# Optimization experiments

Hardware: AMD Instinct MI355X
Metric: run time of the kernel (lower is better)

Reference implementation:

```python
import jax, jax.numpy as jnp
import numpy as np
from jax import lax

B_SZ, L, D, N = 4, 2048, 768, 16


def setup_inputs() -> dict:
    key = jax.random.key(0)
    ks = jax.random.split(key, 8)
    x = jax.random.normal(ks[0], (B_SZ, L, D), dtype=jnp.float32)
    # A_log init: log(repeat(arange(1, N+1), 'n -> d n'))
    A_log = jnp.log(jnp.tile(jnp.arange(1, N + 1, dtype=jnp.float32), (D, 1)))  # (D, N)
    sD = 1.0 / np.sqrt(D)
    Wb = jax.random.normal(ks[1], (N, D), dtype=jnp.float32) * sD
    bb = jax.random.normal(ks[2], (N,), dtype=jnp.float32) * sD
    Wc = jax.random.normal(ks[3], (N, D), dtype=jnp.float32) * sD
    bc = jax.random.normal(ks[4], (N,), dtype=jnp.float32) * sD
    W1 = jax.random.normal(ks[5], (1, D), dtype=jnp.float32) * sD
    b1 = jnp.zeros((1,), dtype=jnp.float32)
    Wd = jax.random.normal(ks[6], (D, 1), dtype=jnp.float32)
    bd = jax.random.normal(ks[7], (D,), dtype=jnp.float32)
    return {"x": x, "A_log": A_log, "Wb": Wb, "bb": bb, "Wc": Wc, "bc": bc,
            "W1": W1, "b1": b1, "Wd": Wd, "bd": bd}


def reference(x, A_log, Wb, bb, Wc, bc, W1, b1, Wd, bd):
    # x: (b, l, d)
    A = -jnp.exp(A_log)                                   # (d, n)
    Bp = x @ Wb.T + bb                                    # (b, l, n)
    C = x @ Wc.T + bc                                     # (b, l, n)
    s1 = x @ W1.T + b1                                    # (b, l, 1)
    delta = jax.nn.softplus(s1 @ Wd.T + bd)               # (b, l, d)
    deltaA = jnp.exp(jnp.einsum('bld,dn->bldn', delta, A))          # (b, l, d, n)
    deltaB_u = jnp.einsum('bld,bln,bld->bldn', delta, Bp, x)        # (b, l, d, n)

    def step(h, inputs):
        dA, dBu, c = inputs                               # (b,d,n),(b,d,n),(b,n)
        h = dA * h + dBu
        y = jnp.einsum('bdn,bn->bd', h, c)
        return h, y

    b, l, d = x.shape
    n = A_log.shape[1]
    h0 = jnp.zeros((b, d, n), dtype=x.dtype)
    _, ys = lax.scan(step, h0, (jnp.moveaxis(deltaA, 1, 0),
                                jnp.moveaxis(deltaB_u, 1, 0),
                                jnp.moveaxis(C, 1, 0)))
    return jnp.moveaxis(ys, 0, 1)                          # (b, l, d)
```

## Files before the change

kernel.cpp:

```cpp
#include <hip/hip_runtime.h>
#include <math.h>

#define B_SZ 4
#define LSEQ 2048
#define DDIM 768
#define NST  16
#define NROW (B_SZ * LSEQ)
#define NJ   33

#define KSPLIT 16
#define KCHUNK (DDIM / KSPLIT)

__global__ __launch_bounds__(256) void proj_part_kernel(
    const float* __restrict__ x,
    const float* __restrict__ Wb, const float* __restrict__ Wc,
    const float* __restrict__ W1, float* __restrict__ part)
{
    __shared__ float xs[256 * (KCHUNK + 1)];
    const int tid = threadIdx.x;
    const int row0 = blockIdx.x * 256;
    const int s = blockIdx.y;
    const int k0 = s * KCHUNK;

    for (int i = tid; i < 256 * (KCHUNK / 4); i += 256) {
        const int r = i / (KCHUNK / 4);
        const int kq = i % (KCHUNK / 4);
        const float4 v = *(const float4*)(x + (size_t)(row0 + r) * DDIM + k0 + kq * 4);
        float* dst = xs + r * (KCHUNK + 1) + kq * 4;
        dst[0] = v.x; dst[1] = v.y; dst[2] = v.z; dst[3] = v.w;
    }
    __syncthreads();

    float xr[KCHUNK];
    #pragma unroll
    for (int k = 0; k < KCHUNK; ++k) xr[k] = xs[tid * (KCHUNK + 1) + k];

    float acc[NJ];
    #pragma unroll
    for (int j = 0; j < NJ; ++j) acc[j] = 0.f;

    #pragma unroll
    for (int j = 0; j < NJ; ++j) {
        const float* wr = (j < 16) ? (Wb + j * DDIM)
                        : (j < 32) ? (Wc + (j - 16) * DDIM)
                                   : W1;
        const float* wk = wr + k0;
        #pragma unroll
        for (int k = 0; k < KCHUNK; ++k) acc[j] = fmaf(xr[k], wk[k], acc[j]);
    }
    #pragma unroll
    for (int j = 0; j < NJ; ++j)
        part[((size_t)s * NJ + j) * NROW + row0 + tid] = acc[j];
}

__global__ __launch_bounds__(256) void proj_reduce_kernel(
    const float* __restrict__ part,
    const float* __restrict__ bb, const float* __restrict__ bc,
    const float* __restrict__ b1,
    float* __restrict__ Bp, float* __restrict__ Cc, float* __restrict__ s1)
{
    const int idx = blockIdx.x * 256 + threadIdx.x;
    const int j = idx / NROW;
    const int row = idx % NROW;
    float a = 0.f;
    #pragma unroll
    for (int s = 0; s < KSPLIT; ++s)
        a += part[((size_t)s * NJ + j) * NROW + row];
    if (j < 16)      Bp[(size_t)row * NST + j] = a + bb[j];
    else if (j < 32) Cc[(size_t)row * NST + (j - 16)] = a + bc[j - 16];
    else             s1[row] = a + b1[0];
}

__device__ __forceinline__ float softplus_f(float z) {
    float t = __expf(-fabsf(z));
    return fmaxf(z, 0.f) + __logf(1.f + t);
}

__device__ __forceinline__ void powers16(float p, float* e) {
    e[0] = p;      e[1] = p * p;      e[2] = e[1] * p;   e[3] = e[1] * e[1];
    e[4] = e[3] * p;  e[5] = e[3] * e[1];  e[6] = e[3] * e[2];  e[7] = e[3] * e[3];
    e[8] = e[7] * p;  e[9] = e[7] * e[1];  e[10] = e[7] * e[2]; e[11] = e[7] * e[3];
    e[12] = e[7] * e[4]; e[13] = e[7] * e[5]; e[14] = e[7] * e[6]; e[15] = e[7] * e[7];
}

__device__ __forceinline__ bool a_structured(const float* acoef) {
    bool st = true;
    #pragma unroll
    for (int n = 0; n < NST; ++n)
        st = st && (fabsf(acoef[n] - (float)(n + 1) * acoef[0]) <= 1e-5f * fabsf(acoef[n]));
    return __all(st) != 0;
}

template <int CS>
__global__ __launch_bounds__(256) void pass1_kernel(
    const float* __restrict__ x, const float* __restrict__ A_log,
    const float* __restrict__ Wd, const float* __restrict__ bd,
    const float* __restrict__ Bp, const float* __restrict__ s1,
    float* __restrict__ Ssum, float* __restrict__ Q)
{
    const int tid = threadIdx.x;
    const int d = blockIdx.x * 256 + tid;
    const int c = blockIdx.y, b = blockIdx.z;
    const int NC = gridDim.y;
    const int rowbase = b * LSEQ + c * CS;

    const float wd = Wd[d], bdv = bd[d];
    float acoef[NST];
    #pragma unroll
    for (int n = 0; n < NST; ++n) acoef[n] = -__expf(A_log[d * NST + n]);
    const float a0 = acoef[0];
    const bool structured = a_structured(acoef);

    const float4* B4 = (const float4*)(Bp + (size_t)rowbase * NST);
    const float* s1p = s1 + rowbase;
    const float* xp = x + (size_t)rowbase * DDIM + d;

    float h[NST];
    #pragma unroll
    for (int n = 0; n < NST; ++n) h[n] = 0.f;
    float S = 0.f;

    if (structured) {
        #pragma unroll 4
        for (int l = 0; l < CS; ++l) {
            const float delta = softplus_f(fmaf(s1p[l], wd, bdv));
            S += delta;
            float e[NST];
            powers16(__expf(delta * a0), e);
            const float dx = delta * xp[(size_t)l * DDIM];
            const float4 b0 = B4[l * 4 + 0], b1v = B4[l * 4 + 1];
            const float4 b2 = B4[l * 4 + 2], b3v = B4[l * 4 + 3];
            const float bv[NST] = {b0.x, b0.y, b0.z, b0.w, b1v.x, b1v.y, b1v.z, b1v.w,
                                   b2.x, b2.y, b2.z, b2.w, b3v.x, b3v.y, b3v.z, b3v.w};
            #pragma unroll
            for (int n = 0; n < NST; ++n) h[n] = fmaf(e[n], h[n], dx * bv[n]);
        }
    } else {
        #pragma unroll 4
        for (int l = 0; l < CS; ++l) {
            const float delta = softplus_f(fmaf(s1p[l], wd, bdv));
            S += delta;
            float e[NST];
            #pragma unroll
            for (int n = 0; n < NST; ++n) e[n] = __expf(delta * acoef[n]);
            const float dx = delta * xp[(size_t)l * DDIM];
            const float4 b0 = B4[l * 4 + 0], b1v = B4[l * 4 + 1];
            const float4 b2 = B4[l * 4 + 2], b3v = B4[l * 4 + 3];
            const float bv[NST] = {b0.x, b0.y, b0.z, b0.w, b1v.x, b1v.y, b1v.z, b1v.w,
                                   b2.x, b2.y, b2.z, b2.w, b3v.x, b3v.y, b3v.z, b3v.w};
            #pragma unroll
            for (int n = 0; n < NST; ++n) h[n] = fmaf(e[n], h[n], dx * bv[n]);
        }
    }
    Ssum[((size_t)b * NC + c) * DDIM + d] = S;
    const size_t gbase = (((size_t)b * NC + c) * DDIM + d) * NST;
    float4* Q4 = (float4*)(Q + gbase);
    #pragma unroll
    for (int q = 0; q < 4; ++q)
        Q4[q] = make_float4(h[q * 4], h[q * 4 + 1], h[q * 4 + 2], h[q * 4 + 3]);
}

__global__ __launch_bounds__(64) void combine_kernel(
    const float* __restrict__ A_log,
    const float* __restrict__ Ssum, const float* __restrict__ Q,
    float* __restrict__ Hin, int NC)
{
    const int idx = blockIdx.x * 64 + threadIdx.x;
    const int b = idx / (DDIM * NST);
    const int r = idx % (DDIM * NST);
    const int d = r / NST;
    const float acoef = -__expf(A_log[r]);
    float h = 0.f;
    #pragma unroll 4
    for (int c = 0; c < NC; ++c) {
        const size_t base = (size_t)(b * NC + c);
        const float Sg = Ssum[base * DDIM + d];
        const float qg = Q[base * (DDIM * NST) + r];
        Hin[base * (DDIM * NST) + r] = h;
        h = fmaf(__expf(acoef * Sg), h, qg);
    }
}

template <int CS>
__global__ __launch_bounds__(256) void pass2_kernel(
    const float* __restrict__ x, const float* __restrict__ A_log,
    const float* __restrict__ Wd, const float* __restrict__ bd,
    const float* __restrict__ Bp, const float* __restrict__ Cc,
    const float* __restrict__ s1, const float* __restrict__ Hin,
    float* __restrict__ out)
{
    const int tid = threadIdx.x;
    const int d = blockIdx.x * 256 + tid;
    const int c = blockIdx.y, b = blockIdx.z;
    const int NC = gridDim.y;
    const int rowbase = b * LSEQ + c * CS;

    const float wd = Wd[d], bdv = bd[d];
    float acoef[NST];
    #pragma unroll
    for (int n = 0; n < NST; ++n) acoef[n] = -__expf(A_log[d * NST + n]);
    const float a0 = acoef[0];
    const bool structured = a_structured(acoef);

    const float4* B4 = (const float4*)(Bp + (size_t)rowbase * NST);
    const float4* C4 = (const float4*)(Cc + (size_t)rowbase * NST);
    const float* s1p = s1 + rowbase;
    const float* xp = x + (size_t)rowbase * DDIM + d;
    float* yp = out + (size_t)rowbase * DDIM + d;

    float h[NST];
    const size_t gbase = (((size_t)b * NC + c) * DDIM + d) * NST;
    const float4* H4 = (const float4*)(Hin + gbase);
    #pragma unroll
    for (int q = 0; q < 4; ++q) {
        const float4 hv = H4[q];
        h[q * 4] = hv.x; h[q * 4 + 1] = hv.y; h[q * 4 + 2] = hv.z; h[q * 4 + 3] = hv.w;
    }

    if (structured) {
        #pragma unroll 4
        for (int l = 0; l < CS; ++l) {
            const float delta = softplus_f(fmaf(s1p[l], wd, bdv));
            float e[NST];
            powers16(__expf(delta * a0), e);
            const float dx = delta * xp[(size_t)l * DDIM];
            const float4 b0 = B4[l * 4 + 0], b1v = B4[l * 4 + 1];
            const float4 b2 = B4[l * 4 + 2], b3v = B4[l * 4 + 3];
            const float4 c0 = C4[l * 4 + 0], c1v = C4[l * 4 + 1];
            const float4 c2 = C4[l * 4 + 2], c3v = C4[l * 4 + 3];
            const float bv[NST] = {b0.x, b0.y, b0.z, b0.w, b1v.x, b1v.y, b1v.z, b1v.w,
                                   b2.x, b2.y, b2.z, b2.w, b3v.x, b3v.y, b3v.z, b3v.w};
            const float cv[NST] = {c0.x, c0.y, c0.z, c0.w, c1v.x, c1v.y, c1v.z, c1v.w,
                                   c2.x, c2.y, c2.z, c2.w, c3v.x, c3v.y, c3v.z, c3v.w};
            float y = 0.f;
            #pragma unroll
            for (int n = 0; n < NST; ++n) {
                h[n] = fmaf(e[n], h[n], dx * bv[n]);
                y = fmaf(h[n], cv[n], y);
            }
            yp[(size_t)l * DDIM] = y;
        }
    } else {
        #pragma unroll 4
        for (int l = 0; l < CS; ++l) {
            const float delta = softplus_f(fmaf(s1p[l], wd, bdv));
            float e[NST];
            #pragma unroll
            for (int n = 0; n < NST; ++n) e[n] = __expf(delta * acoef[n]);
            const float dx = delta * xp[(size_t)l * DDIM];
            const float4 b0 = B4[l * 4 + 0], b1v = B4[l * 4 + 1];
            const float4 b2 = B4[l * 4 + 2], b3v = B4[l * 4 + 3];
            const float4 c0 = C4[l * 4 + 0], c1v = C4[l * 4 + 1];
            const float4 c2 = C4[l * 4 + 2], c3v = C4[l * 4 + 3];
            const float bv[NST] = {b0.x, b0.y, b0.z, b0.w, b1v.x, b1v.y, b1v.z, b1v.w,
                                   b2.x, b2.y, b2.z, b2.w, b3v.x, b3v.y, b3v.z, b3v.w};
            const float cv[NST] = {c0.x, c0.y, c0.z, c0.w, c1v.x, c1v.y, c1v.z, c1v.w,
                                   c2.x, c2.y, c2.z, c2.w, c3v.x, c3v.y, c3v.z, c3v.w};
            float y = 0.f;
            #pragma unroll
            for (int n = 0; n < NST; ++n) {
                h[n] = fmaf(e[n], h[n], dx * bv[n]);
                y = fmaf(h[n], cv[n], y);
            }
            yp[(size_t)l * DDIM] = y;
        }
    }
}

extern "C" void kernel_launch(void* const* d_in, const int* in_sizes, int n_in,
                              void* d_out, int out_size, void* d_ws, size_t ws_size,
                              hipStream_t stream) {
    const float* x     = (const float*)d_in[0];
    const float* A_log = (const float*)d_in[1];
    const float* Wb    = (const float*)d_in[2];
    const float* bb    = (const float*)d_in[3];
    const float* Wc    = (const float*)d_in[4];
    const float* bc    = (const float*)d_in[5];
    const float* W1    = (const float*)d_in[6];
    const float* b1    = (const float*)d_in[7];
    const float* Wd    = (const float*)d_in[8];
    const float* bd    = (const float*)d_in[9];
    float* out = (float*)d_out;

    float* ws = (float*)d_ws;
    const size_t partN = (size_t)KSPLIT * NJ * NROW;
    const size_t BpN = (size_t)NROW * NST;
    const size_t s1N = (size_t)NROW;

    int NC = 64;
    while (NC > 16) {
        size_t agg_ = (size_t)B_SZ * NC * DDIM * NST;
        size_t sN_ = (size_t)B_SZ * NC * DDIM;
        size_t need = (partN + 2 * BpN + s1N + sN_ + 2 * agg_) * sizeof(float);
        if (need <= ws_size) break;
        NC >>= 1;
    }
    const int CS = LSEQ / NC;

    float* part = ws;
    float* Bp   = part + partN;
    float* Cc   = Bp + BpN;
    float* s1   = Cc + BpN;
    float* Ssum = s1 + s1N;
    const size_t sN = (size_t)B_SZ * NC * DDIM;
    const size_t agg = (size_t)B_SZ * NC * DDIM * NST;
    float* Q    = Ssum + sN;
    float* Hin  = Q + agg;

    dim3 gproj(NROW / 256, KSPLIT);
    proj_part_kernel<<<gproj, 256, 0, stream>>>(x, Wb, Wc, W1, part);
    proj_reduce_kernel<<<(NJ * NROW) / 256, 256, 0, stream>>>(part, bb, bc, b1, Bp, Cc, s1);

    dim3 gscan(DDIM / 256, NC, B_SZ);
    if (CS == 32)
        pass1_kernel<32><<<gscan, 256, 0, stream>>>(x, A_log, Wd, bd, Bp, s1, Ssum, Q);
    else if (CS == 64)
        pass1_kernel<64><<<gscan, 256, 0, stream>>>(x, A_log, Wd, bd, Bp, s1, Ssum, Q);
    else
        pass1_kernel<128><<<gscan, 256, 0, stream>>>(x, A_log, Wd, bd, Bp, s1, Ssum, Q);

    combine_kernel<<<(B_SZ * DDIM * NST) / 64, 64, 0, stream>>>(A_log, Ssum, Q, Hin, NC);

    if (CS == 32)
        pass2_kernel<32><<<gscan, 256, 0, stream>>>(x, A_log, Wd, bd, Bp, Cc, s1, Hin, out);
    else if (CS == 64)
        pass2_kernel<64><<<gscan, 256, 0, stream>>>(x, A_log, Wd, bd, Bp, Cc, s1, Hin, out);
    else
        pass2_kernel<128><<<gscan, 256, 0, stream>>>(x, A_log, Wd, bd, Bp, Cc, s1, Hin, out);
}
```

Baseline: 160.6 us.

## Restructure projection GEMM split and parallelize chunk-carry combine with wave shuffles

The projection kernel now uses 64-row tiles with a 4-way K split, and each wave computes a subset of the 33 output columns. Before, each thread held 48 x values and all 33 accumulators, so register pressure was high and the partial-sum buffer was large. The combine kernel splits the 64 chunks across 4 lane groups, computes group products and carries, scans them with shuffles, and then writes Hin. This replaces a serial 64-step loop per state. The number of chunks is also fixed at 64 at compile time, which drops the workspace-size fallback and the template dispatch, so a smaller workspace would no longer be handled.

```diff
diff --git a/kernel.cpp b/kernel.cpp
--- a/kernel.cpp
+++ b/kernel.cpp
@@ -8,49 +8,63 @@
 #define NROW (B_SZ * LSEQ)
 #define NJ   33
 
-#define KSPLIT 16
-#define KCHUNK (DDIM / KSPLIT)
+#define NC   64
+#define CS   (LSEQ / NC)
+
+#define RB    64
+#define KSPL  4
+#define KC    (DDIM / KSPL)
 
 __global__ __launch_bounds__(256) void proj_part_kernel(
     const float* __restrict__ x,
     const float* __restrict__ Wb, const float* __restrict__ Wc,
     const float* __restrict__ W1, float* __restrict__ part)
 {
-    __shared__ float xs[256 * (KCHUNK + 1)];
+    __shared__ float xs[RB * (KC + 1)];
     const int tid = threadIdx.x;
-    const int row0 = blockIdx.x * 256;
+    const int row0 = blockIdx.x * RB;
     const int s = blockIdx.y;
-    const int k0 = s * KCHUNK;
-
-    for (int i = tid; i < 256 * (KCHUNK / 4); i += 256) {
-        const int r = i / (KCHUNK / 4);
-        const int kq = i % (KCHUNK / 4);
+    const int k0 = s * KC;
+
+    for (int i = tid; i < RB * (KC / 4); i += 256) {
+        const int r = i / (KC / 4);
+        const int kq = i % (KC / 4);
         const float4 v = *(const float4*)(x + (size_t)(row0 + r) * DDIM + k0 + kq * 4);
-        float* dst = xs + r * (KCHUNK + 1) + kq * 4;
+        float* dst = xs + r * (KC + 1) + kq * 4;
         dst[0] = v.x; dst[1] = v.y; dst[2] = v.z; dst[3] = v.w;
     }
     __syncthreads();
 
-    float xr[KCHUNK];
-    #pragma unroll
-    for (int k = 0; k < KCHUNK; ++k) xr[k] = xs[tid * (KCHUNK + 1) + k];
-
-    float acc[NJ];
-    #pragma unroll
-    for (int j = 0; j < NJ; ++j) acc[j] = 0.f;
-
-    #pragma unroll
-    for (int j = 0; j < NJ; ++j) {
+    const int row = tid & 63;
+    const int jg = __builtin_amdgcn_readfirstlane(tid >> 6);
+
+    const float* wp[9];
+    #pragma unroll
+    for (int t = 0; t < 9; ++t) {
+        const int j = 4 * t + jg;
         const float* wr = (j < 16) ? (Wb + j * DDIM)
                         : (j < 32) ? (Wc + (j - 16) * DDIM)
                                    : W1;
-        const float* wk = wr + k0;
+        wp[t] = wr + k0;
+    }
+    float acc[9];
+    #pragma unroll
+    for (int t = 0; t < 9; ++t) acc[t] = 0.f;
+
+    const float* xr = xs + row * (KC + 1);
+    #pragma unroll 8
+    for (int k = 0; k < KC; ++k) {
+        const float xv = xr[k];
         #pragma unroll
-        for (int k = 0; k < KCHUNK; ++k) acc[j] = fmaf(xr[k], wk[k], acc[j]);
-    }
-    #pragma unroll
-    for (int j = 0; j < NJ; ++j)
-        part[((size_t)s * NJ + j) * NROW + row0 + tid] = acc[j];
+        for (int t = 0; t < 9; ++t)
+            if (4 * t + jg < 33) acc[t] = fmaf(xv, wp[t][k], acc[t]);
+    }
+    #pragma unroll
+    for (int t = 0; t < 9; ++t) {
+        const int j = 4 * t + jg;
+        if (j < 33)
+            part[((size_t)s * NJ + j) * NROW + row0 + row] = acc[t];
+    }
 }
 
 __global__ __launch_bounds__(256) void proj_reduce_kernel(
@@ -64,7 +78,7 @@
     const int row = idx % NROW;
     float a = 0.f;
     #pragma unroll
-    for (int s = 0; s < KSPLIT; ++s)
+    for (int s = 0; s < KSPL; ++s)
         a += part[((size_t)s * NJ + j) * NROW + row];
     if (j < 16)      Bp[(size_t)row * NST + j] = a + bb[j];
     else if (j < 32) Cc[(size_t)row * NST + (j - 16)] = a + bc[j - 16];
@@ -91,7 +105,6 @@
     return __all(st) != 0;
 }
 
-template <int CS>
 __global__ __launch_bounds__(256) void pass1_kernel(
     const float* __restrict__ x, const float* __restrict__ A_log,
     const float* __restrict__ Wd, const float* __restrict__ bd,
@@ -101,7 +114,6 @@
     const int tid = threadIdx.x;
     const int d = blockIdx.x * 256 + tid;
     const int c = blockIdx.y, b = blockIdx.z;
-    const int NC = gridDim.y;
     const int rowbase = b * LSEQ + c * CS;
 
     const float wd = Wd[d], bdv = bd[d];
@@ -160,28 +172,54 @@
         Q4[q] = make_float4(h[q * 4], h[q * 4 + 1], h[q * 4 + 2], h[q * 4 + 3]);
 }
 
-__global__ __launch_bounds__(64) void combine_kernel(
+#define CPG (NC / 4)
+__global__ __launch_bounds__(256) void combine_kernel(
     const float* __restrict__ A_log,
     const float* __restrict__ Ssum, const float* __restrict__ Q,
-    float* __restrict__ Hin, int NC)
-{
-    const int idx = blockIdx.x * 64 + threadIdx.x;
-    const int b = idx / (DDIM * NST);
-    const int r = idx % (DDIM * NST);
-    const int d = r / NST;
+    float* __restrict__ Hin)
+{
+    const int gidx = blockIdx.x * 256 + threadIdx.x;
+    const int lane = threadIdx.x & 63;
+    const int rlow = gidx & 15;
+    const int g = (gidx >> 4) & 3;
+    const int hi = gidx >> 6;
+    const int pairIdx = hi * 16 + rlow;
+    const int b = pairIdx / (DDIM * NST);
+    const int r = pairIdx % (DDIM * NST);
+    const int d = r >> 4;
     const float acoef = -__expf(A_log[r]);
-    float h = 0.f;
-    #pragma unroll 4
-    for (int c = 0; c < NC; ++c) {
-        const size_t base = (size_t)(b * NC + c);
-        const float Sg = Ssum[base * DDIM + d];
-        const float qg = Q[base * (DDIM * NST) + r];
+    const int c0 = g * CPG;
+
+    float eq[CPG], qq[CPG];
+    #pragma unroll
+    for (int ci = 0; ci < CPG; ++ci) {
+        const size_t base = (size_t)(b * NC + c0 + ci);
+        eq[ci] = __expf(acoef * Ssum[base * DDIM + d]);
+        qq[ci] = Q[base * (DDIM * NST) + r];
+    }
+    float E = 1.f, H = 0.f;
+    #pragma unroll
+    for (int ci = 0; ci < CPG; ++ci) { H = fmaf(eq[ci], H, qq[ci]); E *= eq[ci]; }
+
+    float oE = __shfl_up(E, 16, 64);
+    float oH = __shfl_up(H, 16, 64);
+    if (lane >= 16) { H = fmaf(E, oH, H); E *= oE; }
+    oE = __shfl_up(E, 32, 64);
+    oH = __shfl_up(H, 32, 64);
+    if (lane >= 32) { H = fmaf(E, oH, H); E *= oE; }
+
+    float hin = __shfl_up(H, 16, 64);
+    if (g == 0) hin = 0.f;
+
+    float h = hin;
+    #pragma unroll
+    for (int ci = 0; ci < CPG; ++ci) {
+        const size_t base = (size_t)(b * NC + c0 + ci);
         Hin[base * (DDIM * NST) + r] = h;
-        h = fmaf(__expf(acoef * Sg), h, qg);
-    }
-}
-
-template <int CS>
+        h = fmaf(eq[ci], h, qq[ci]);
+    }
+}
+
 __global__ __launch_bounds__(256) void pass2_kernel(
     const float* __restrict__ x, const float* __restrict__ A_log,
     const float* __restrict__ Wd, const float* __restrict__ bd,
@@ -192,7 +230,6 @@
     const int tid = threadIdx.x;
     const int d = blockIdx.x * 256 + tid;
     const int c = blockIdx.y, b = blockIdx.z;
-    const int NC = gridDim.y;
     const int rowbase = b * LSEQ + c * CS;
 
     const float wd = Wd[d], bdv = bd[d];
@@ -283,48 +320,28 @@
     float* out = (float*)d_out;
 
     float* ws = (float*)d_ws;
-    const size_t partN = (size_t)KSPLIT * NJ * NROW;
+    const size_t partN = (size_t)KSPL * NJ * NROW;
     const size_t BpN = (size_t)NROW * NST;
     const size_t s1N = (size_t)NROW;
-
-    int NC = 64;
-    while (NC > 16) {
-        size_t agg_ = (size_t)B_SZ * NC * DDIM * NST;
-        size_t sN_ = (size_t)B_SZ * NC * DDIM;
-        size_t need = (partN + 2 * BpN + s1N + sN_ + 2 * agg_) * sizeof(float);
-        if (need <= ws_size) break;
-        NC >>= 1;
-    }
-    const int CS = LSEQ / NC;
+    const size_t sN  = (size_t)B_SZ * NC * DDIM;
+    const size_t agg = (size_t)B_SZ * NC * DDIM * NST;
 
     float* part = ws;
     float* Bp   = part + partN;
     float* Cc   = Bp + BpN;
     float* s1   = Cc + BpN;
     float* Ssum = s1 + s1N;
-    const size_t sN = (size_t)B_SZ * NC * DDIM;
-    const size_t agg = (size_t)B_SZ * NC * DDIM * NST;
     float* Q    = Ssum + sN;
     float* Hin  = Q + agg;
 
-    dim3 gproj(NROW / 256, KSPLIT);
+    dim3 gproj(NROW / RB, KSPL);
     proj_part_kernel<<<gproj, 256, 0, stream>>>(x, Wb, Wc, W1, part);
     proj_reduce_kernel<<<(NJ * NROW) / 256, 256, 0, stream>>>(part, bb, bc, b1, Bp, Cc, s1);
 
     dim3 gscan(DDIM / 256, NC, B_SZ);
-    if (CS == 32)
-        pass1_kernel<32><<<gscan, 256, 0, stream>>>(x, A_log, Wd, bd, Bp, s1, Ssum, Q);
-    else if (CS == 64)
-        pass1_kernel<64><<<gscan, 256, 0, stream>>>(x, A_log, Wd, bd, Bp, s1, Ssum, Q);
-    else
-        pass1_kernel<128><<<gscan, 256, 0, stream>>>(x, A_log, Wd, bd, Bp, s1, Ssum, Q);
-
-    combine_kernel<<<(B_SZ * DDIM * NST) / 64, 64, 0, stream>>>(A_log, Ssum, Q, Hin, NC);
-
-    if (CS == 32)
-        pass2_kernel<32><<<gscan, 256, 0, stream>>>(x, A_log, Wd, bd, Bp, Cc, s1, Hin, out);
-    else if (CS == 64)
-        pass2_kernel<64><<<gscan, 256, 0, stream>>>(x, A_log, Wd, bd, Bp, Cc, s1, Hin, out);
-    else
-        pass2_kernel<128><<<gscan, 256, 0, stream>>>(x, A_log, Wd, bd, Bp, Cc, s1, Hin, out);
-}
+    pass1_kernel<<<gscan, 256, 0, stream>>>(x, A_log, Wd, bd, Bp, s1, Ssum, Q);
+
+    combine_kernel<<<(B_SZ * DDIM * NST * 4) / 256, 256, 0, stream>>>(A_log, Ssum, Q, Hin);
+
+    pass2_kernel<<<gscan, 256, 0, stream>>>(x, A_log, Wd, bd, Bp, Cc, s1, Hin, out);
+}
```

Result: slower. 219.1 us (+36.4%).
